# Performance work log

Measured on AMD Instinct MI355X. Metric: run time of the kernel, lower is better.

Reference implementation:

```python
import jax, jax.numpy as jnp
import numpy as np
import math

D_MODEL = 1024
D_HEAD = 64
BATCH = 8
SEQ = 2048


def setup_inputs() -> dict:
    key = jax.random.key(0)
    ks = jax.random.split(key, 5)
    s = 0.02
    return {
        "residual_stream": jax.random.normal(ks[0], (BATCH, SEQ, D_MODEL), dtype=jnp.float32),
        "Wq": jax.random.normal(ks[1], (D_HEAD, D_MODEL), dtype=jnp.float32) * s,
        "Wk": jax.random.normal(ks[2], (D_HEAD, D_MODEL), dtype=jnp.float32) * s,
        "Wv": jax.random.normal(ks[3], (D_HEAD, D_MODEL), dtype=jnp.float32) * s,
        "Wo": jax.random.normal(ks[4], (D_MODEL, D_HEAD), dtype=jnp.float32) * s,
    }


def reference(residual_stream, Wq, Wk, Wv, Wo):
    # NOTE: module scales by 1/sqrt(d_model), NOT 1/sqrt(d_head)
    scale = 1.0 / math.sqrt(D_MODEL)
    q = jnp.einsum('bsd,hd->bsh', residual_stream, Wq)  # [B,S,Dh]
    k = jnp.einsum('bsd,hd->bsh', residual_stream, Wk)  # [B,S,Dh]
    scores = jnp.einsum('bqh,bkh->bqk', q, k) * scale   # [B,S,S]
    seq = scores.shape[-1]
    causal = jnp.tril(jnp.ones((seq, seq), dtype=bool))
    scores = jnp.where(causal[None, :, :], scores, jnp.float32(-jnp.inf))
    attn = jax.nn.softmax(scores, axis=-1)
    # O applied to V *before* the attention-weighted sum (as in the module)
    x = jnp.einsum('bsh,dh->bsd', jnp.einsum('bsd,hd->bsh', residual_stream, Wv), Wo)  # [B,S,Dm]
    return jnp.einsum('bqk,bkd->bqd', attn, x)
```

## Files before the change

### kernel.cpp

```cpp
#include <hip/hip_runtime.h>

#define SEQ 2048
#define DMODEL 1024
#define DHEAD 64
#define NROWS 16384
#define ATT_SC2 0.0450842300667f

typedef __attribute__((ext_vector_type(8))) short bf16x8;
typedef __attribute__((ext_vector_type(4))) float f32x4;
typedef __attribute__((ext_vector_type(4))) unsigned int u32x4;
typedef __attribute__((ext_vector_type(4))) unsigned short u16x4;
typedef __attribute__((ext_vector_type(4))) float fl4;

#define MFMA16(a,b,c) __builtin_amdgcn_mfma_f32_16x16x32_bf16((a),(b),(c),0,0,0)
#define GLL16(g, l) __builtin_amdgcn_global_load_lds( \
    (const __attribute__((address_space(1))) void*)(g), \
    (__attribute__((address_space(3))) void*)(l), 16, 0, 0)

__device__ __forceinline__ unsigned short f2bf(float f) {
    union { float f; unsigned int u; } v; v.f = f;
    unsigned int u = v.u;
    unsigned int r = u + 0x7fffu + ((u >> 16) & 1u);
    return (unsigned short)(r >> 16);
}

__device__ __forceinline__ unsigned int cvtpk(float lo, float hi) {
    unsigned int d;
    asm volatile("v_cvt_pk_bf16_f32 %0, %1, %2" : "=v"(d) : "v"(lo), "v"(hi));
    return d;
}

__global__ __launch_bounds__(256) void k_cvt(
    const float* __restrict__ Wq, const float* __restrict__ Wk,
    const float* __restrict__ Wv, const float* __restrict__ Wo,
    unsigned short* __restrict__ Wb,
    unsigned short* __restrict__ Wob)
{
    int i4 = blockIdx.x * 256 + threadIdx.x;
    const int W1 = 16384;
    const float* src; unsigned short* dst; int off;
    if (i4 < 3 * W1) {
        int which = i4 / W1;
        off = i4 - which * W1;
        src = (which == 0) ? Wq : (which == 1) ? Wk : Wv;
        dst = Wb + (size_t)which * 65536;
    } else {
        off = i4 - 3 * W1; src = Wo; dst = Wob;
    }
    fl4 v = reinterpret_cast<const fl4*>(src)[off];
    u16x4 o;
    o[0] = f2bf(v[0]); o[1] = f2bf(v[1]); o[2] = f2bf(v[2]); o[3] = f2bf(v[3]);
    reinterpret_cast<u16x4*>(dst)[off] = o;
}

__global__ __launch_bounds__(256) void k_qkv(
    const float* __restrict__ x,
    const unsigned short* __restrict__ Wb,
    unsigned short* __restrict__ Qb,
    unsigned short* __restrict__ Kb,
    unsigned short* __restrict__ Vt)
{
    __shared__ __align__(16) char smem[81920];

    int tid = threadIdx.x;
    int wave = tid >> 6, lane = tid & 63, g = lane >> 4, lr = lane & 15;
    int mbase = blockIdx.x * 64;

    const float* xsrc[4];
#pragma unroll
    for (int j = 0; j < 4; ++j) {
        int ci = (wave * 4 + j) * 64 + lane;
        int row = ci >> 4, c = ci & 15, cg = c ^ (row & 7);
        xsrc[j] = x + (size_t)(mbase + row) * DMODEL + cg * 4;
    }
    const unsigned short* wsrc[6];
#pragma unroll
    for (int j = 0; j < 6; ++j) {
        int ci = (wave * 6 + j) * 64 + lane;
        int row = ci >> 3, c = ci & 7, cg = c ^ (row & 7);
        wsrc[j] = Wb + (size_t)row * DMODEL + cg * 8;
    }

    f32x4 acc[12];
#pragma unroll
    for (int f = 0; f < 12; ++f) acc[f] = (f32x4){0.f, 0.f, 0.f, 0.f};

#pragma unroll
    for (int j = 0; j < 4; ++j) GLL16(xsrc[j], smem + (wave * 4 + j) * 1024);
#pragma unroll
    for (int j = 0; j < 6; ++j) GLL16(wsrc[j], smem + 32768 + (wave * 6 + j) * 1024);

    for (int ks = 0; ks < 16; ++ks) {
        int cur = ks & 1;
        if (ks < 15) {
            int nb = cur ^ 1;
#pragma unroll
            for (int j = 0; j < 4; ++j)
                GLL16(xsrc[j] + (ks + 1) * 64, smem + nb * 16384 + (wave * 4 + j) * 1024);
#pragma unroll
            for (int j = 0; j < 6; ++j)
                GLL16(wsrc[j] + (ks + 1) * 64, smem + 32768 + nb * 24576 + (wave * 6 + j) * 1024);
            asm volatile("s_waitcnt vmcnt(10)" ::: "memory");
        } else {
            asm volatile("s_waitcnt vmcnt(0)" ::: "memory");
        }
        __builtin_amdgcn_s_barrier();
        asm volatile("" ::: "memory");

        const float* Xf = (const float*)(smem + cur * 16384);
        const unsigned short* Wf = (const unsigned short*)(smem + 32768 + cur * 24576);
        int arow = wave * 16 + lr;
#pragma unroll
        for (int kc = 0; kc < 2; ++kc) {
            int c0 = (kc * 8 + g * 2) ^ (lr & 7);
            int c1 = (kc * 8 + g * 2 + 1) ^ (lr & 7);
            fl4 xa = *(const fl4*)&Xf[arow * 64 + c0 * 4];
            fl4 xb = *(const fl4*)&Xf[arow * 64 + c1 * 4];
            union { unsigned int u[4]; bf16x8 v; } a;
            a.u[0] = cvtpk(xa[0], xa[1]); a.u[1] = cvtpk(xa[2], xa[3]);
            a.u[2] = cvtpk(xb[0], xb[1]); a.u[3] = cvtpk(xb[2], xb[3]);
            __builtin_amdgcn_s_setprio(1);
#pragma unroll
            for (int f = 0; f < 12; ++f) {
                int brow = f * 16 + lr;
                int cb = (kc * 4 + g) ^ (lr & 7);
                bf16x8 b = *(const bf16x8*)&Wf[brow * 64 + cb * 8];
                acc[f] = MFMA16(a.v, b, acc[f]);
            }
            __builtin_amdgcn_s_setprio(0);
        }
        asm volatile("" ::: "memory");
        __builtin_amdgcn_s_barrier();
    }

    int mrow = mbase + wave * 16 + g * 4;
#pragma unroll
    for (int f = 0; f < 8; ++f) {
        int col = f * 16 + lr;
#pragma unroll
        for (int r = 0; r < 4; ++r) {
            unsigned short bv = f2bf(acc[f][r]);
            if (f < 4) Qb[(size_t)(mrow + r) * DHEAD + col] = bv;
            else       Kb[(size_t)(mrow + r) * DHEAD + col - 64] = bv;
        }
    }
    unsigned short* tmp = (unsigned short*)smem;
#pragma unroll
    for (int f = 8; f < 12; ++f) {
        int h = (f - 8) * 16 + lr;
#pragma unroll
        for (int r = 0; r < 4; ++r)
            tmp[(wave * 16 + g * 4 + r) * 72 + h] = f2bf(acc[f][r]);
    }
    __syncthreads();
    int b = mbase >> 11, sbase = mbase & 2047;
    int h = tid >> 2, sc = tid & 3;
    u32x4 o0, o1;
#pragma unroll
    for (int j = 0; j < 4; ++j) {
        o0[j] = (unsigned int)tmp[(sc * 16 + 2 * j) * 72 + h] |
                ((unsigned int)tmp[(sc * 16 + 2 * j + 1) * 72 + h] << 16);
        o1[j] = (unsigned int)tmp[(sc * 16 + 8 + 2 * j) * 72 + h] |
                ((unsigned int)tmp[(sc * 16 + 9 + 2 * j) * 72 + h] << 16);
    }
    size_t off = ((size_t)(b * 64 + h)) * SEQ + sbase + sc * 16;
    *reinterpret_cast<u32x4*>(&Vt[off]) = o0;
    *reinterpret_cast<u32x4*>(&Vt[off + 8]) = o1;
}

__global__ __launch_bounds__(256) void k_attn(
    const unsigned short* __restrict__ Qb,
    const unsigned short* __restrict__ Kb,
    const unsigned short* __restrict__ Vt,
    float* __restrict__ Op,
    float* __restrict__ Lp)
{
    __shared__ __align__(16) char smem[40960];

    int tid = threadIdx.x;
    int wave = tid >> 6, lane = tid & 63, g = lane >> 4, lr = lane & 15;
    int bid = blockIdx.x;
    int qt = 31 - (bid >> 4);
    int sub = bid & 15;
    int b = sub >> 1, chunk = sub & 1;
    int nt = qt + 1;
    int my_nt = (nt + 1 - chunk) >> 1;
    int qw = qt * 64 + wave * 16;
    size_t qrowbase = (size_t)(b * SEQ) + qw;

    bf16x8 aq[2];
#pragma unroll
    for (int kc = 0; kc < 2; ++kc)
        aq[kc] = *reinterpret_cast<const bf16x8*>(
            &Qb[(qrowbase + lr) * DHEAD + kc * 32 + g * 8]);

    const unsigned short* ksrc[2];
    const unsigned short* vsrc[2];
#pragma unroll
    for (int j = 0; j < 2; ++j) {
        int ci = j * 256 + tid;
        int row = ci >> 3, c = ci & 7, cg = c ^ (row & 7);
        ksrc[j] = Kb + ((size_t)(b * SEQ) + row) * DHEAD + cg * 8;
        vsrc[j] = Vt + ((size_t)(b * DHEAD) + row) * SEQ + cg * 8;
    }

    float l_part[4];
    f32x4 of[4];
#pragma unroll
    for (int r = 0; r < 4; ++r) l_part[r] = 0.f;
#pragma unroll
    for (int f = 0; f < 4; ++f) of[f] = (f32x4){0.f, 0.f, 0.f, 0.f};

    if (my_nt > 0) {
#pragma unroll
        for (int j = 0; j < 2; ++j)
            GLL16(ksrc[j] + (size_t)chunk * 64 * DHEAD, smem + j * 4096 + wave * 1024);
#pragma unroll
        for (int j = 0; j < 2; ++j)
            GLL16(vsrc[j] + chunk * 64, smem + 16384 + j * 4096 + wave * 1024);

        for (int i = 0; i < my_nt; ++i) {
            int t = chunk + 2 * i;
            int cur = i & 1;
            int kvb = t * 64;
            if (i + 1 < my_nt) {
                int nb = cur ^ 1;
#pragma unroll
                for (int j = 0; j < 2; ++j)
                    GLL16(ksrc[j] + (size_t)(t + 2) * 64 * DHEAD,
                          smem + nb * 8192 + j * 4096 + wave * 1024);
#pragma unroll
                for (int j = 0; j < 2; ++j)
                    GLL16(vsrc[j] + (t + 2) * 64,
                          smem + 16384 + nb * 8192 + j * 4096 + wave * 1024);
                asm volatile("s_waitcnt vmcnt(4)" ::: "memory");
            } else {
                asm volatile("s_waitcnt vmcnt(0)" ::: "memory");
            }
            __builtin_amdgcn_s_barrier();
            asm volatile("" ::: "memory");

            if (kvb <= qw + 15) {
                const unsigned short* Kl = (const unsigned short*)(smem + cur * 8192);
                const unsigned short* Vl = (const unsigned short*)(smem + 16384 + cur * 8192);
                unsigned short* Pl = (unsigned short*)(smem + 32768) + wave * 1024;

                f32x4 s[4];
#pragma unroll
                for (int f = 0; f < 4; ++f) s[f] = (f32x4){0.f, 0.f, 0.f, 0.f};
                __builtin_amdgcn_s_setprio(1);
#pragma unroll
                for (int kc = 0; kc < 2; ++kc) {
#pragma unroll
                    for (int f = 0; f < 4; ++f) {
                        int brow = f * 16 + lr;
                        int cb = (kc * 4 + g) ^ (lr & 7);
                        bf16x8 bk = *(const bf16x8*)&Kl[brow * 64 + cb * 8];
                        s[f] = MFMA16(aq[kc], bk, s[f]);
                    }
                }
                __builtin_amdgcn_s_setprio(0);

                if (kvb + 63 <= qw) {
#pragma unroll
                    for (int f = 0; f < 4; ++f)
#pragma unroll
                        for (int r = 0; r < 4; ++r) {
                            float p = exp2f(s[f][r] * ATT_SC2);
                            s[f][r] = p;
                            l_part[r] += p;
                        }
                } else {
#pragma unroll
                    for (int f = 0; f < 4; ++f) {
                        int kvg = kvb + f * 16 + lr;
#pragma unroll
                        for (int r = 0; r < 4; ++r) {
                            int qr = qw + g * 4 + r;
                            float p = exp2f(s[f][r] * ATT_SC2);
                            p = (kvg > qr) ? 0.f : p;
                            s[f][r] = p;
                            l_part[r] += p;
                        }
                    }
                }
#pragma unroll
                for (int f = 0; f < 4; ++f) {
#pragma unroll
                    for (int r = 0; r < 4; ++r) {
                        int row = g * 4 + r, col = f * 16 + lr;
                        int ch = (col >> 3) ^ (row & 7);
                        Pl[row * 64 + ch * 8 + (col & 7)] = f2bf(s[f][r]);
                    }
                }
#pragma unroll
                for (int kc = 0; kc < 2; ++kc) {
                    int cp = (kc * 4 + g) ^ (lr & 7);
                    bf16x8 ap = *(const bf16x8*)&Pl[lr * 64 + cp * 8];
                    __builtin_amdgcn_s_setprio(1);
#pragma unroll
                    for (int fd = 0; fd < 4; ++fd) {
                        int vrow = fd * 16 + lr;
                        int cv = (kc * 4 + g) ^ (lr & 7);
                        bf16x8 bv = *(const bf16x8*)&Vl[vrow * 64 + cv * 8];
                        of[fd] = MFMA16(ap, bv, of[fd]);
                    }
                    __builtin_amdgcn_s_setprio(0);
                }
            }
            asm volatile("" ::: "memory");
            __builtin_amdgcn_s_barrier();
        }
    }

    float* opb = Op + ((size_t)chunk * NROWS + qrowbase) * 64;
#pragma unroll
    for (int r = 0; r < 4; ++r) {
        float ls = l_part[r];
        ls += __shfl_xor(ls, 1); ls += __shfl_xor(ls, 2);
        ls += __shfl_xor(ls, 4); ls += __shfl_xor(ls, 8);
        if (lr == 0)
            Lp[(size_t)chunk * NROWS + qrowbase + g * 4 + r] = ls;
#pragma unroll
        for (int fd = 0; fd < 4; ++fd)
            opb[(g * 4 + r) * 64 + fd * 16 + lr] = of[fd][r];
    }
}

__global__ __launch_bounds__(256) void k_oproj(
    const float* __restrict__ Op,
    const float* __restrict__ Lp,
    const unsigned short* __restrict__ Wob,
    float* __restrict__ out)
{
    __shared__ __align__(16) unsigned short Wl[256 * 64];
    int tid = threadIdx.x;
    int wave = tid >> 6, lane = tid & 63, g = lane >> 4, lr = lane & 15;
    int mb = blockIdx.x * 64, nb = blockIdx.y * 256;

#pragma unroll
    for (int p = 0; p < 8; ++p) {
        int idx = p * 256 + tid;
        int row = idx >> 3, c = idx & 7;
        int ch = c ^ (row & 7);
        u32x4 v = *reinterpret_cast<const u32x4*>(
            &Wob[(size_t)(nb + row) * DHEAD + c * 8]);
        *reinterpret_cast<u32x4*>(&Wl[row * 64 + ch * 8]) = v;
    }
    __syncthreads();

    int row = mb + wave * 16 + lr;
    float inv = 1.0f / (Lp[row] + Lp[NROWS + row]);
    bf16x8 ao[2];
#pragma unroll
    for (int kc = 0; kc < 2; ++kc) {
        const float* p0 = &Op[(size_t)row * 64 + kc * 32 + g * 8];
        const float* p1 = &Op[(size_t)(NROWS + row) * 64 + kc * 32 + g * 8];
        fl4 a0 = *(const fl4*)p0, b0 = *(const fl4*)(p0 + 4);
        fl4 a1 = *(const fl4*)p1, b1 = *(const fl4*)(p1 + 4);
        union { unsigned int u[4]; bf16x8 v; } a;
        a.u[0] = cvtpk((a0[0] + a1[0]) * inv, (a0[1] + a1[1]) * inv);
        a.u[1] = cvtpk((a0[2] + a1[2]) * inv, (a0[3] + a1[3]) * inv);
        a.u[2] = cvtpk((b0[0] + b1[0]) * inv, (b0[1] + b1[1]) * inv);
        a.u[3] = cvtpk((b0[2] + b1[2]) * inv, (b0[3] + b1[3]) * inv);
        ao[kc] = a.v;
    }

    f32x4 acc[16];
#pragma unroll
    for (int f = 0; f < 16; ++f) acc[f] = (f32x4){0.f, 0.f, 0.f, 0.f};
#pragma unroll
    for (int kc = 0; kc < 2; ++kc) {
        __builtin_amdgcn_s_setprio(1);
#pragma unroll
        for (int f = 0; f < 16; ++f) {
            int brow = f * 16 + lr;
            int cb = (kc * 4 + g) ^ (brow & 7);
            bf16x8 bw = *reinterpret_cast<const bf16x8*>(&Wl[brow * 64 + cb * 8]);
            acc[f] = MFMA16(ao[kc], bw, acc[f]);
        }
        __builtin_amdgcn_s_setprio(0);
    }
    int mrow = mb + wave * 16 + g * 4;
#pragma unroll
    for (int f = 0; f < 16; ++f) {
#pragma unroll
        for (int r = 0; r < 4; ++r)
            out[(size_t)(mrow + r) * DMODEL + nb + f * 16 + lr] = acc[f][r];
    }
}

extern "C" void kernel_launch(void* const* d_in, const int* in_sizes, int n_in,
                              void* d_out, int out_size, void* d_ws, size_t ws_size,
                              hipStream_t stream) {
    const float* x  = (const float*)d_in[0];
    const float* Wq = (const float*)d_in[1];
    const float* Wk = (const float*)d_in[2];
    const float* Wv = (const float*)d_in[3];
    const float* Wo = (const float*)d_in[4];
    float* out = (float*)d_out;

    unsigned short* Wb  = (unsigned short*)d_ws;
    unsigned short* Wob = Wb + 196608;
    unsigned short* Qb  = Wob + 65536;
    unsigned short* Kb  = Qb + 1048576;
    unsigned short* Vt  = Kb + 1048576;
    float* Op = (float*)(Vt + 1048576);
    float* Lp = Op + 2 * NROWS * 64;

    k_cvt<<<256, 256, 0, stream>>>(Wq, Wk, Wv, Wo, Wb, Wob);
    k_qkv<<<256, 256, 0, stream>>>(x, Wb, Qb, Kb, Vt);
    k_attn<<<512, 256, 0, stream>>>(Qb, Kb, Vt, Op, Lp);
    k_oproj<<<dim3(256, 4), 256, 0, stream>>>(Op, Lp, Wob, out);
}
```

Before: 66.47 us.

## Split attention KV range into four chunks and combine partials in output projection

The attention kernel now splits each query tile's causal KV range into four interleaved chunks instead of two, and launches 1024 blocks instead of 512. Odd chunks walk the query tiles in reverse order to balance the causal workload. The output projection kernel sums four partial outputs and denominators before normalising. This is meant to raise parallelism and shorten the longest-running blocks, at the cost of twice the partial-result traffic and more prologue overhead per block.

```diff
diff --git a/kernel.cpp b/kernel.cpp
--- a/kernel.cpp
+++ b/kernel.cpp
@@ -180,11 +180,12 @@
     int tid = threadIdx.x;
     int wave = tid >> 6, lane = tid & 63, g = lane >> 4, lr = lane & 15;
     int bid = blockIdx.x;
-    int qt = 31 - (bid >> 4);
-    int sub = bid & 15;
-    int b = sub >> 1, chunk = sub & 1;
-    int nt = qt + 1;
-    int my_nt = (nt + 1 - chunk) >> 1;
+    int chunk = bid >> 8;
+    int idx = bid & 255;
+    int hv = idx >> 3;
+    int qt = (chunk & 1) ? hv : 31 - hv;
+    int b = idx & 7;
+    int my_nt = (qt >= chunk) ? ((qt - chunk) >> 2) + 1 : 0;
     int qw = qt * 64 + wave * 16;
     size_t qrowbase = (size_t)(b * SEQ) + qw;
 
@@ -220,18 +221,18 @@
             GLL16(vsrc[j] + chunk * 64, smem + 16384 + j * 4096 + wave * 1024);
 
         for (int i = 0; i < my_nt; ++i) {
-            int t = chunk + 2 * i;
+            int t = chunk + 4 * i;
             int cur = i & 1;
             int kvb = t * 64;
             if (i + 1 < my_nt) {
                 int nb = cur ^ 1;
 #pragma unroll
                 for (int j = 0; j < 2; ++j)
-                    GLL16(ksrc[j] + (size_t)(t + 2) * 64 * DHEAD,
+                    GLL16(ksrc[j] + (size_t)(t + 4) * 64 * DHEAD,
                           smem + nb * 8192 + j * 4096 + wave * 1024);
 #pragma unroll
                 for (int j = 0; j < 2; ++j)
-                    GLL16(vsrc[j] + (t + 2) * 64,
+                    GLL16(vsrc[j] + (t + 4) * 64,
                           smem + 16384 + nb * 8192 + j * 4096 + wave * 1024);
                 asm volatile("s_waitcnt vmcnt(4)" ::: "memory");
             } else {
@@ -350,20 +351,27 @@
     __syncthreads();
 
     int row = mb + wave * 16 + lr;
-    float inv = 1.0f / (Lp[row] + Lp[NROWS + row]);
+    float inv = 1.0f / (Lp[row] + Lp[NROWS + row] +
+                        Lp[2 * NROWS + row] + Lp[3 * NROWS + row]);
     bf16x8 ao[2];
 #pragma unroll
     for (int kc = 0; kc < 2; ++kc) {
-        const float* p0 = &Op[(size_t)row * 64 + kc * 32 + g * 8];
-        const float* p1 = &Op[(size_t)(NROWS + row) * 64 + kc * 32 + g * 8];
-        fl4 a0 = *(const fl4*)p0, b0 = *(const fl4*)(p0 + 4);
-        fl4 a1 = *(const fl4*)p1, b1 = *(const fl4*)(p1 + 4);
-        union { unsigned int u[4]; bf16x8 v; } a;
-        a.u[0] = cvtpk((a0[0] + a1[0]) * inv, (a0[1] + a1[1]) * inv);
-        a.u[1] = cvtpk((a0[2] + a1[2]) * inv, (a0[3] + a1[3]) * inv);
-        a.u[2] = cvtpk((b0[0] + b1[0]) * inv, (b0[1] + b1[1]) * inv);
-        a.u[3] = cvtpk((b0[2] + b1[2]) * inv, (b0[3] + b1[3]) * inv);
-        ao[kc] = a.v;
+        float v[8];
+#pragma unroll
+        for (int j = 0; j < 8; ++j) v[j] = 0.f;
+#pragma unroll
+        for (int c = 0; c < 4; ++c) {
+            const float* p = &Op[((size_t)c * NROWS + row) * 64 + kc * 32 + g * 8];
+            fl4 a = *(const fl4*)p, bq = *(const fl4*)(p + 4);
+#pragma unroll
+            for (int j = 0; j < 4; ++j) { v[j] += a[j]; v[j + 4] += bq[j]; }
+        }
+        union { unsigned int u[4]; bf16x8 w; } a;
+        a.u[0] = cvtpk(v[0] * inv, v[1] * inv);
+        a.u[1] = cvtpk(v[2] * inv, v[3] * inv);
+        a.u[2] = cvtpk(v[4] * inv, v[5] * inv);
+        a.u[3] = cvtpk(v[6] * inv, v[7] * inv);
+        ao[kc] = a.w;
     }
 
     f32x4 acc[16];
@@ -406,10 +414,10 @@
     unsigned short* Kb  = Qb + 1048576;
     unsigned short* Vt  = Kb + 1048576;
     float* Op = (float*)(Vt + 1048576);
-    float* Lp = Op + 2 * NROWS * 64;
+    float* Lp = Op + 4 * NROWS * 64;
 
     k_cvt<<<256, 256, 0, stream>>>(Wq, Wk, Wv, Wo, Wb, Wob);
     k_qkv<<<256, 256, 0, stream>>>(x, Wb, Qb, Kb, Vt);
-    k_attn<<<512, 256, 0, stream>>>(Qb, Kb, Vt, Op, Lp);
+    k_attn<<<1024, 256, 0, stream>>>(Qb, Kb, Vt, Op, Lp);
     k_oproj<<<dim3(256, 4), 256, 0, stream>>>(Op, Lp, Wob, out);
 }
```

After: 69.70 us. +4.9%, slower.

## Fuse attention and output projection into one kernel with paired q-tile balancing

Applied to the files above, without the earlier changes.

Merges the attention and Wo-projection kernels. Each block handles a pair of 32-row q-tiles (pid and 63-pid) so causal work is balanced across blocks. Within a block, two wave pairs split the KV tiles and their partial outputs are combined through LDS. The normalized result is then multiplied by Wo read directly from global memory, and the second tile's K/V prefetch is issued before the projection. This removes the fp32 partial-output round trip and a kernel launch, but the grid shrinks to 256 blocks and LDS use grows to 72KB, which may reduce occupancy.

```diff
diff --git a/kernel.cpp b/kernel.cpp
--- a/kernel.cpp
+++ b/kernel.cpp
@@ -168,31 +168,19 @@
     *reinterpret_cast<u32x4*>(&Vt[off + 8]) = o1;
 }
 
-__global__ __launch_bounds__(256) void k_attn(
+__global__ __launch_bounds__(256) void k_fused(
     const unsigned short* __restrict__ Qb,
     const unsigned short* __restrict__ Kb,
     const unsigned short* __restrict__ Vt,
-    float* __restrict__ Op,
-    float* __restrict__ Lp)
+    const unsigned short* __restrict__ Wob,
+    float* __restrict__ out)
 {
-    __shared__ __align__(16) char smem[40960];
+    __shared__ __align__(16) char smem[73728];
 
     int tid = threadIdx.x;
     int wave = tid >> 6, lane = tid & 63, g = lane >> 4, lr = lane & 15;
-    int bid = blockIdx.x;
-    int qt = 31 - (bid >> 4);
-    int sub = bid & 15;
-    int b = sub >> 1, chunk = sub & 1;
-    int nt = qt + 1;
-    int my_nt = (nt + 1 - chunk) >> 1;
-    int qw = qt * 64 + wave * 16;
-    size_t qrowbase = (size_t)(b * SEQ) + qw;
-
-    bf16x8 aq[2];
-#pragma unroll
-    for (int kc = 0; kc < 2; ++kc)
-        aq[kc] = *reinterpret_cast<const bf16x8*>(
-            &Qb[(qrowbase + lr) * DHEAD + kc * 32 + g * 8]);
+    int pair = wave >> 1, pw = wave & 1;
+    int pid = blockIdx.x, b = blockIdx.y;
 
     const unsigned short* ksrc[2];
     const unsigned short* vsrc[2];
@@ -204,50 +192,60 @@
         vsrc[j] = Vt + ((size_t)(b * DHEAD) + row) * SEQ + cg * 8;
     }
 
-    float l_part[4];
-    f32x4 of[4];
-#pragma unroll
-    for (int r = 0; r < 4; ++r) l_part[r] = 0.f;
-#pragma unroll
-    for (int f = 0; f < 4; ++f) of[f] = (f32x4){0.f, 0.f, 0.f, 0.f};
-
-    if (my_nt > 0) {
-#pragma unroll
-        for (int j = 0; j < 2; ++j)
-            GLL16(ksrc[j] + (size_t)chunk * 64 * DHEAD, smem + j * 4096 + wave * 1024);
-#pragma unroll
-        for (int j = 0; j < 2; ++j)
-            GLL16(vsrc[j] + chunk * 64, smem + 16384 + j * 4096 + wave * 1024);
-
-        for (int i = 0; i < my_nt; ++i) {
-            int t = chunk + 2 * i;
-            int cur = i & 1;
-            int kvb = t * 64;
-            if (i + 1 < my_nt) {
-                int nb = cur ^ 1;
-#pragma unroll
-                for (int j = 0; j < 2; ++j)
-                    GLL16(ksrc[j] + (size_t)(t + 2) * 64 * DHEAD,
-                          smem + nb * 8192 + j * 4096 + wave * 1024);
-#pragma unroll
-                for (int j = 0; j < 2; ++j)
-                    GLL16(vsrc[j] + (t + 2) * 64,
-                          smem + 16384 + nb * 8192 + j * 4096 + wave * 1024);
-                asm volatile("s_waitcnt vmcnt(4)" ::: "memory");
+#define STAGE(n_, s_) do {                                                   \
+    int te_ = (2 * (s_)) * 64;                                               \
+    int to_ = ((2 * (s_) + 1 < (n_)) ? (2 * (s_) + 1) : ((n_) - 1)) * 64;    \
+    char* base_ = smem + ((s_) & 1) * 32768;                                 \
+    _Pragma("unroll")                                                        \
+    for (int j_ = 0; j_ < 2; ++j_) {                                         \
+        GLL16(ksrc[j_] + (size_t)te_ * DHEAD, base_ + j_ * 4096 + wave * 1024);          \
+        GLL16(ksrc[j_] + (size_t)to_ * DHEAD, base_ + 8192 + j_ * 4096 + wave * 1024);   \
+        GLL16(vsrc[j_] + te_, base_ + 16384 + j_ * 4096 + wave * 1024);                  \
+        GLL16(vsrc[j_] + to_, base_ + 24576 + j_ * 4096 + wave * 1024);                  \
+    } } while (0)
+
+    for (int ql = 0; ql < 2; ++ql) {
+        int qt = ql ? (63 - pid) : pid;
+        int n = (qt >> 1) + 1;
+        int nsteps = (n + 1) >> 1;
+        int qw = qt * 32 + pw * 16;
+        size_t qrowbase = (size_t)(b * SEQ) + qw;
+
+        bf16x8 aq[2];
+#pragma unroll
+        for (int kc = 0; kc < 2; ++kc)
+            aq[kc] = *(const bf16x8*)&Qb[(qrowbase + lr) * DHEAD + kc * 32 + g * 8];
+
+        if (ql == 0) STAGE(n, 0);
+
+        float l_part[4];
+        f32x4 of[4];
+#pragma unroll
+        for (int r = 0; r < 4; ++r) l_part[r] = 0.f;
+#pragma unroll
+        for (int f = 0; f < 4; ++f) of[f] = (f32x4){0.f, 0.f, 0.f, 0.f};
+
+        for (int s = 0; s < nsteps; ++s) {
+            if (s + 1 < nsteps) {
+                STAGE(n, s + 1);
+                asm volatile("s_waitcnt vmcnt(8)" ::: "memory");
             } else {
                 asm volatile("s_waitcnt vmcnt(0)" ::: "memory");
             }
             __builtin_amdgcn_s_barrier();
             asm volatile("" ::: "memory");
 
-            if (kvb <= qw + 15) {
-                const unsigned short* Kl = (const unsigned short*)(smem + cur * 8192);
-                const unsigned short* Vl = (const unsigned short*)(smem + 16384 + cur * 8192);
-                unsigned short* Pl = (unsigned short*)(smem + 32768) + wave * 1024;
-
-                f32x4 s[4];
-#pragma unroll
-                for (int f = 0; f < 4; ++f) s[f] = (f32x4){0.f, 0.f, 0.f, 0.f};
+            int t = 2 * s + pair, kvb = t * 64;
+            if (t < n && kvb <= qw + 15) {
+                const unsigned short* Kl =
+                    (const unsigned short*)(smem + (s & 1) * 32768 + pair * 8192);
+                const unsigned short* Vl =
+                    (const unsigned short*)(smem + (s & 1) * 32768 + 16384 + pair * 8192);
+                unsigned short* Pl = (unsigned short*)(smem + 65536) + wave * 1024;
+
+                f32x4 s4[4];
+#pragma unroll
+                for (int f = 0; f < 4; ++f) s4[f] = (f32x4){0.f, 0.f, 0.f, 0.f};
                 __builtin_amdgcn_s_setprio(1);
 #pragma unroll
                 for (int kc = 0; kc < 2; ++kc) {
@@ -256,7 +254,7 @@
                         int brow = f * 16 + lr;
                         int cb = (kc * 4 + g) ^ (lr & 7);
                         bf16x8 bk = *(const bf16x8*)&Kl[brow * 64 + cb * 8];
-                        s[f] = MFMA16(aq[kc], bk, s[f]);
+                        s4[f] = MFMA16(aq[kc], bk, s4[f]);
                     }
                 }
                 __builtin_amdgcn_s_setprio(0);
@@ -266,8 +264,8 @@
                     for (int f = 0; f < 4; ++f)
 #pragma unroll
                         for (int r = 0; r < 4; ++r) {
-                            float p = exp2f(s[f][r] * ATT_SC2);
-                            s[f][r] = p;
+                            float p = exp2f(s4[f][r] * ATT_SC2);
+                            s4[f][r] = p;
                             l_part[r] += p;
                         }
                 } else {
@@ -277,9 +275,9 @@
 #pragma unroll
                         for (int r = 0; r < 4; ++r) {
                             int qr = qw + g * 4 + r;
-                            float p = exp2f(s[f][r] * ATT_SC2);
+                            float p = exp2f(s4[f][r] * ATT_SC2);
                             p = (kvg > qr) ? 0.f : p;
-                            s[f][r] = p;
+                            s4[f][r] = p;
                             l_part[r] += p;
                         }
                     }
@@ -290,7 +288,7 @@
                     for (int r = 0; r < 4; ++r) {
                         int row = g * 4 + r, col = f * 16 + lr;
                         int ch = (col >> 3) ^ (row & 7);
-                        Pl[row * 64 + ch * 8 + (col & 7)] = f2bf(s[f][r]);
+                        Pl[row * 64 + ch * 8 + (col & 7)] = f2bf(s4[f][r]);
                     }
                 }
 #pragma unroll
@@ -311,83 +309,87 @@
             asm volatile("" ::: "memory");
             __builtin_amdgcn_s_barrier();
         }
-    }
-
-    float* opb = Op + ((size_t)chunk * NROWS + qrowbase) * 64;
-#pragma unroll
-    for (int r = 0; r < 4; ++r) {
-        float ls = l_part[r];
-        ls += __shfl_xor(ls, 1); ls += __shfl_xor(ls, 2);
-        ls += __shfl_xor(ls, 4); ls += __shfl_xor(ls, 8);
-        if (lr == 0)
-            Lp[(size_t)chunk * NROWS + qrowbase + g * 4 + r] = ls;
-#pragma unroll
-        for (int fd = 0; fd < 4; ++fd)
-            opb[(g * 4 + r) * 64 + fd * 16 + lr] = of[fd][r];
-    }
-}
-
-__global__ __launch_bounds__(256) void k_oproj(
-    const float* __restrict__ Op,
-    const float* __restrict__ Lp,
-    const unsigned short* __restrict__ Wob,
-    float* __restrict__ out)
-{
-    __shared__ __align__(16) unsigned short Wl[256 * 64];
-    int tid = threadIdx.x;
-    int wave = tid >> 6, lane = tid & 63, g = lane >> 4, lr = lane & 15;
-    int mb = blockIdx.x * 64, nb = blockIdx.y * 256;
-
-#pragma unroll
-    for (int p = 0; p < 8; ++p) {
-        int idx = p * 256 + tid;
-        int row = idx >> 3, c = idx & 7;
-        int ch = c ^ (row & 7);
-        u32x4 v = *reinterpret_cast<const u32x4*>(
-            &Wob[(size_t)(nb + row) * DHEAD + c * 8]);
-        *reinterpret_cast<u32x4*>(&Wl[row * 64 + ch * 8]) = v;
-    }
-    __syncthreads();
-
-    int row = mb + wave * 16 + lr;
-    float inv = 1.0f / (Lp[row] + Lp[NROWS + row]);
-    bf16x8 ao[2];
-#pragma unroll
-    for (int kc = 0; kc < 2; ++kc) {
-        const float* p0 = &Op[(size_t)row * 64 + kc * 32 + g * 8];
-        const float* p1 = &Op[(size_t)(NROWS + row) * 64 + kc * 32 + g * 8];
-        fl4 a0 = *(const fl4*)p0, b0 = *(const fl4*)(p0 + 4);
-        fl4 a1 = *(const fl4*)p1, b1 = *(const fl4*)(p1 + 4);
-        union { unsigned int u[4]; bf16x8 v; } a;
-        a.u[0] = cvtpk((a0[0] + a1[0]) * inv, (a0[1] + a1[1]) * inv);
-        a.u[1] = cvtpk((a0[2] + a1[2]) * inv, (a0[3] + a1[3]) * inv);
-        a.u[2] = cvtpk((b0[0] + b1[0]) * inv, (b0[1] + b1[1]) * inv);
-        a.u[3] = cvtpk((b0[2] + b1[2]) * inv, (b0[3] + b1[3]) * inv);
-        ao[kc] = a.v;
-    }
-
-    f32x4 acc[16];
-#pragma unroll
-    for (int f = 0; f < 16; ++f) acc[f] = (f32x4){0.f, 0.f, 0.f, 0.f};
-#pragma unroll
-    for (int kc = 0; kc < 2; ++kc) {
-        __builtin_amdgcn_s_setprio(1);
-#pragma unroll
-        for (int f = 0; f < 16; ++f) {
-            int brow = f * 16 + lr;
-            int cb = (kc * 4 + g) ^ (brow & 7);
-            bf16x8 bw = *reinterpret_cast<const bf16x8*>(&Wl[brow * 64 + cb * 8]);
-            acc[f] = MFMA16(ao[kc], bw, acc[f]);
-        }
-        __builtin_amdgcn_s_setprio(0);
-    }
-    int mrow = mb + wave * 16 + g * 4;
-#pragma unroll
-    for (int f = 0; f < 16; ++f) {
-#pragma unroll
-        for (int r = 0; r < 4; ++r)
-            out[(size_t)(mrow + r) * DMODEL + nb + f * 16 + lr] = acc[f][r];
-    }
+
+        {
+            float* Obuf = (float*)(smem + pair * 8704);
+            float* Ol = (float*)(smem + 17408);
+            int row32 = pw * 16 + g * 4;
+#pragma unroll
+            for (int r = 0; r < 4; ++r) {
+                float ls = l_part[r];
+                ls += __shfl_xor(ls, 1); ls += __shfl_xor(ls, 2);
+                ls += __shfl_xor(ls, 4); ls += __shfl_xor(ls, 8);
+                if (lr == 0) Ol[pair * 32 + row32 + r] = ls;
+#pragma unroll
+                for (int fd = 0; fd < 4; ++fd)
+                    Obuf[(row32 + r) * 68 + fd * 16 + lr] = of[fd][r];
+            }
+        }
+        __syncthreads();
+
+        bf16x8 ao[2][2];
+        {
+            const float* O0 = (const float*)smem;
+            const float* O1 = (const float*)(smem + 8704);
+            const float* Ol = (const float*)(smem + 17408);
+#pragma unroll
+            for (int m = 0; m < 2; ++m) {
+                int arow = m * 16 + lr;
+                float inv = 1.f / (Ol[arow] + Ol[32 + arow]);
+#pragma unroll
+                for (int kc = 0; kc < 2; ++kc) {
+                    int cb = arow * 68 + kc * 32 + g * 8;
+                    fl4 xa = *(const fl4*)&O0[cb], xb = *(const fl4*)&O0[cb + 4];
+                    fl4 ya = *(const fl4*)&O1[cb], yb = *(const fl4*)&O1[cb + 4];
+                    union { unsigned int u[4]; bf16x8 v; } a;
+                    a.u[0] = cvtpk((xa[0] + ya[0]) * inv, (xa[1] + ya[1]) * inv);
+                    a.u[1] = cvtpk((xa[2] + ya[2]) * inv, (xa[3] + ya[3]) * inv);
+                    a.u[2] = cvtpk((xb[0] + yb[0]) * inv, (xb[1] + yb[1]) * inv);
+                    a.u[3] = cvtpk((xb[2] + yb[2]) * inv, (xb[3] + yb[3]) * inv);
+                    ao[m][kc] = a.v;
+                }
+            }
+        }
+        __syncthreads();
+
+        if (ql == 0) {
+            int qt2 = 63 - pid;
+            int n2 = (qt2 >> 1) + 1;
+            STAGE(n2, 0);
+        }
+
+        {
+            int nb = wave * 256;
+            f32x4 acc[2][16];
+#pragma unroll
+            for (int m = 0; m < 2; ++m)
+#pragma unroll
+                for (int f = 0; f < 16; ++f) acc[m][f] = (f32x4){0.f, 0.f, 0.f, 0.f};
+#pragma unroll
+            for (int kc = 0; kc < 2; ++kc) {
+                __builtin_amdgcn_s_setprio(1);
+#pragma unroll
+                for (int f = 0; f < 16; ++f) {
+                    bf16x8 bw = *(const bf16x8*)
+                        &Wob[(size_t)(nb + f * 16 + lr) * DHEAD + kc * 32 + g * 8];
+                    acc[0][f] = MFMA16(ao[0][kc], bw, acc[0][f]);
+                    acc[1][f] = MFMA16(ao[1][kc], bw, acc[1][f]);
+                }
+                __builtin_amdgcn_s_setprio(0);
+            }
+            int mb = b * SEQ + qt * 32;
+#pragma unroll
+            for (int m = 0; m < 2; ++m) {
+                int mrow = mb + m * 16 + g * 4;
+#pragma unroll
+                for (int f = 0; f < 16; ++f)
+#pragma unroll
+                    for (int r = 0; r < 4; ++r)
+                        out[(size_t)(mrow + r) * DMODEL + nb + f * 16 + lr] = acc[m][f][r];
+            }
+        }
+    }
+#undef STAGE
 }
 
 extern "C" void kernel_launch(void* const* d_in, const int* in_sizes, int n_in,
@@ -405,11 +407,8 @@
     unsigned short* Qb  = Wob + 65536;
     unsigned short* Kb  = Qb + 1048576;
     unsigned short* Vt  = Kb + 1048576;
-    float* Op = (float*)(Vt + 1048576);
-    float* Lp = Op + 2 * NROWS * 64;
 
     k_cvt<<<256, 256, 0, stream>>>(Wq, Wk, Wv, Wo, Wb, Wob);
     k_qkv<<<256, 256, 0, stream>>>(x, Wb, Qb, Kb, Vt);
-    k_attn<<<512, 256, 0, stream>>>(Qb, Kb, Vt, Op, Lp);
-    k_oproj<<<dim3(256, 4), 256, 0, stream>>>(Op, Lp, Wob, out);
-}
+    k_fused<<<dim3(32, 8), 256, 0, stream>>>(Qb, Kb, Vt, Wob, out);
+}
```

After: 67.63 us. No clear change (+1.7%).
